# Performance work log

Hardware: AMD Instinct MI355X
Metric: run time of the kernel (lower is better)

Reference implementation:

```python
import jax, jax.numpy as jnp
import numpy as np

BS, SEQ, C, NC, H, W = 8, 512, 512, 5, 768, 768


def setup_inputs() -> dict:
    key = jax.random.key(0)
    k1, k2, k3, k4, k5, k6, k7, k8 = jax.random.split(key, 8)
    fuse_embeddings = jax.random.normal(k1, (BS, SEQ, C), dtype=jnp.float32)
    class_labels = jax.random.normal(k2, (BS, NC, H, W), dtype=jnp.float32)
    # valid boxes: x0<x1<=W, y0<y1<=H (coords order: x0, y0, x1, y1)
    x0 = jax.random.randint(k3, (BS, SEQ), 0, W - 1)
    y0 = jax.random.randint(k4, (BS, SEQ), 0, H - 1)
    x1 = jnp.minimum(x0 + jax.random.randint(k5, (BS, SEQ), 1, 64), W)
    y1 = jnp.minimum(y0 + jax.random.randint(k6, (BS, SEQ), 1, 16), H)
    coords = jnp.stack([x0, y0, x1, y1], axis=-1).astype(jnp.int32)
    mask = jax.random.randint(k7, (BS, SEQ), 0, 2).astype(jnp.int32)
    # classification_net (Linear) params
    bound = 1.0 / np.sqrt(C)
    Wc = jax.random.uniform(k8, (NC, C), minval=-bound, maxval=bound, dtype=jnp.float32)
    bc = jnp.zeros((NC,), dtype=jnp.float32)
    return {"fuse_embeddings": fuse_embeddings, "class_labels": class_labels,
            "Wc": Wc, "bc": bc, "coords": coords, "mask": mask}


def _forward(fuse_embeddings, class_labels, Wc, bc, coords, mask):
    bs, seq_len, _ = fuse_embeddings.shape
    nc = Wc.shape[0]
    # linear classifier over all tokens: [bs, seq, nc]
    logits = jnp.einsum("bsc,nc->bsn", fuse_embeddings, Wc) + bc
    # per-pixel hard label: [bs, H, W]
    lab = jnp.argmax(class_labels, axis=1)
    onehot = jax.nn.one_hot(lab, nc, dtype=logits.dtype)  # [bs, H, W, nc]
    # padded integral image -> O(1) box histograms (replaces per-ROI bincount)
    ii = jnp.cumsum(jnp.cumsum(onehot, axis=1), axis=2)
    ii = jnp.pad(ii, ((0, 0), (1, 0), (1, 0), (0, 0)))  # [bs, H+1, W+1, nc]
    x0, y0, x1, y1 = coords[..., 0], coords[..., 1], coords[..., 2], coords[..., 3]
    # degenerate-box fix from the original code
    y1 = jnp.where(y1 == y0, y1 + 1, y1)
    x1 = jnp.where(x1 == x0, x1 + 1, x1)
    b_idx = jnp.arange(bs)[:, None]
    g = lambda y, x: ii[b_idx, y, x, :]
    counts = g(y1, x1) - g(y0, x1) - g(y1, x0) + g(y0, x0)  # [bs, seq, nc]
    maj = jnp.argmax(counts, axis=-1)  # majority-vote label, first-max tiebreak like bincount().argmax()
    # masked-mean cross entropy (CE over tokens with mask==1)
    logp = jax.nn.log_softmax(logits, axis=-1)
    nll = -jnp.take_along_axis(logp, maj[..., None], axis=-1)[..., 0]
    m = (mask == 1).astype(logits.dtype)
    return jnp.sum(nll * m) / jnp.sum(m)


def reference(fuse_embeddings, class_labels, Wc, bc, coords, mask):
    return _forward(fuse_embeddings, class_labels, Wc, bc, coords, mask)
```

## Files before the change

### kernel.cpp

```cpp
#include <hip/hip_runtime.h>

#define BS 8
#define SEQ 512
#define CDIM 512
#define NC 5
#define IMG_H 768
#define IMG_W 768
#define HW (IMG_H * IMG_W)
#define NTOK (BS * SEQ)

__global__ __launch_bounds__(256) void token_kernel(
    const float* __restrict__ emb,
    const float* __restrict__ cls,
    const float* __restrict__ Wc,
    const float* __restrict__ bc,
    const int*   __restrict__ coords,
    const int*   __restrict__ mask,
    float2* __restrict__ ws)
{
    const int token = blockIdx.x;
    const int b     = token / SEQ;
    const int t     = threadIdx.x;
    const int wave  = t >> 6;
    const int lane  = t & 63;

    const float2 e = *(const float2*)(emb + (size_t)token * CDIM + t * 2);
    float part[NC];
#pragma unroll
    for (int c = 0; c < NC; ++c) {
        const float2 w = *(const float2*)(Wc + c * CDIM + t * 2);
        part[c] = e.x * w.x + e.y * w.y;
    }

    int x0 = coords[token * 4 + 0];
    int y0 = coords[token * 4 + 1];
    int x1 = coords[token * 4 + 2];
    int y1 = coords[token * 4 + 3];
    if (y1 == y0) y1++;
    if (x1 == x0) x1++;
    if (x1 > IMG_W) x1 = IMG_W;
    if (y1 > IMG_H) y1 = IMG_H;

    const int tx = lane;
    const int ty = wave;

    int hist[NC] = {0, 0, 0, 0, 0};
    const float* base = cls + (size_t)b * NC * HW;
    for (int yy = y0 + ty; yy < y1; yy += 4) {
        for (int xx = x0 + tx; xx < x1; xx += 64) {
            const float* p = base + yy * IMG_W + xx;
            const float v0 = p[0 * HW];
            const float v1 = p[1 * HW];
            const float v2 = p[2 * HW];
            const float v3 = p[3 * HW];
            const float v4 = p[4 * HW];
            int lab = 0; float best = v0;
            if (v1 > best) { best = v1; lab = 1; }
            if (v2 > best) { best = v2; lab = 2; }
            if (v3 > best) { best = v3; lab = 3; }
            if (v4 > best) { best = v4; lab = 4; }
#pragma unroll
            for (int c = 0; c < NC; ++c) hist[c] += (lab == c);
        }
    }

#pragma unroll
    for (int off = 32; off >= 1; off >>= 1) {
#pragma unroll
        for (int c = 0; c < NC; ++c) {
            part[c] += __shfl_down(part[c], off);
            hist[c] += __shfl_down(hist[c], off);
        }
    }

    __shared__ float s_part[4][NC];
    __shared__ int   s_hist[4][NC];
    if (lane == 0) {
#pragma unroll
        for (int c = 0; c < NC; ++c) {
            s_part[wave][c] = part[c];
            s_hist[wave][c] = hist[c];
        }
    }
    __syncthreads();

    if (t == 0) {
        float l[NC];
        int   h[NC];
#pragma unroll
        for (int c = 0; c < NC; ++c) {
            l[c] = s_part[0][c] + s_part[1][c] + s_part[2][c] + s_part[3][c] + bc[c];
            h[c] = s_hist[0][c] + s_hist[1][c] + s_hist[2][c] + s_hist[3][c];
        }
        int maj = 0, bestc = h[0];
#pragma unroll
        for (int c = 1; c < NC; ++c)
            if (h[c] > bestc) { bestc = h[c]; maj = c; }

        float m = l[0];
#pragma unroll
        for (int c = 1; c < NC; ++c) m = fmaxf(m, l[c]);
        float s = 0.0f;
#pragma unroll
        for (int c = 0; c < NC; ++c) s += __expf(l[c] - m);
        const float nll = m + __logf(s) - l[maj];

        const float mk = (mask[token] == 1) ? 1.0f : 0.0f;
        ws[token] = make_float2(nll * mk, mk);
    }
}

__global__ __launch_bounds__(256) void finalize_kernel(
    const float2* __restrict__ ws, float* __restrict__ out)
{
    float a = 0.0f, bsum = 0.0f;
    for (int i = threadIdx.x; i < NTOK; i += 256) {
        const float2 v = ws[i];
        a += v.x; bsum += v.y;
    }
#pragma unroll
    for (int off = 32; off >= 1; off >>= 1) {
        a    += __shfl_down(a, off);
        bsum += __shfl_down(bsum, off);
    }
    __shared__ float sa[4], sb[4];
    const int wave = threadIdx.x >> 6;
    if ((threadIdx.x & 63) == 0) { sa[wave] = a; sb[wave] = bsum; }
    __syncthreads();
    if (threadIdx.x == 0) {
        a    = sa[0] + sa[1] + sa[2] + sa[3];
        bsum = sb[0] + sb[1] + sb[2] + sb[3];
        out[0] = a / bsum;
    }
}

extern "C" void kernel_launch(void* const* d_in, const int* in_sizes, int n_in,
                              void* d_out, int out_size, void* d_ws, size_t ws_size,
                              hipStream_t stream) {
    const float* emb    = (const float*)d_in[0];
    const float* cls    = (const float*)d_in[1];
    const float* Wc     = (const float*)d_in[2];
    const float* bc     = (const float*)d_in[3];
    const int*   coords = (const int*)d_in[4];
    const int*   mask   = (const int*)d_in[5];
    float* out = (float*)d_out;
    float2* ws = (float2*)d_ws;

    token_kernel<<<NTOK, 256, 0, stream>>>(emb, cls, Wc, bc, coords, mask, ws);
    finalize_kernel<<<1, 256, 0, stream>>>(ws, out);
}
```

Before: 151.3 us.

## Map one wavefront per token and pack histogram into 64-bit counter

Each block now handles four tokens, one per wavefront, instead of one token per 256-thread block. Within a wave, each lane covers one box column (box widths stay below 64) and loops over the rows. The five class counts are packed into 12-bit fields of a single 64-bit value, so the wave reduction needs one shuffle chain instead of five. The per-token logits use wider float4 loads, and partial sums are combined per block, which shrinks the finalize input. The column mapping assumes boxes at most 64 wide and at most 4095 pixels per field.

```diff
diff --git a/kernel.cpp b/kernel.cpp
--- a/kernel.cpp
+++ b/kernel.cpp
@@ -8,6 +8,7 @@
 #define IMG_W 768
 #define HW (IMG_H * IMG_W)
 #define NTOK (BS * SEQ)
+#define NBLK (NTOK / 4)
 
 __global__ __launch_bounds__(256) void token_kernel(
     const float* __restrict__ emb,
@@ -18,19 +19,11 @@
     const int*   __restrict__ mask,
     float2* __restrict__ ws)
 {
-    const int token = blockIdx.x;
-    const int b     = token / SEQ;
     const int t     = threadIdx.x;
     const int wave  = t >> 6;
     const int lane  = t & 63;
-
-    const float2 e = *(const float2*)(emb + (size_t)token * CDIM + t * 2);
-    float part[NC];
-#pragma unroll
-    for (int c = 0; c < NC; ++c) {
-        const float2 w = *(const float2*)(Wc + c * CDIM + t * 2);
-        part[c] = e.x * w.x + e.y * w.y;
-    }
+    const int token = blockIdx.x * 4 + wave;
+    const int b     = token >> 9;
 
     int x0 = coords[token * 4 + 0];
     int y0 = coords[token * 4 + 1];
@@ -41,61 +34,62 @@
     if (x1 > IMG_W) x1 = IMG_W;
     if (y1 > IMG_H) y1 = IMG_H;
 
-    const int tx = lane;
-    const int ty = wave;
+    unsigned long long hp = 0ull;
+    {
+        const int xx = x0 + lane;
+        const bool xok = (xx < x1);
+        const float* p0 = cls + (size_t)b * NC * HW + y0 * IMG_W + xx;
+#pragma unroll 4
+        for (int yy = y0; yy < y1; ++yy, p0 += IMG_W) {
+            if (xok) {
+                const float v0 = p0[0 * HW];
+                const float v1 = p0[1 * HW];
+                const float v2 = p0[2 * HW];
+                const float v3 = p0[3 * HW];
+                const float v4 = p0[4 * HW];
+                int lab = 0; float best = v0;
+                if (v1 > best) { best = v1; lab = 1; }
+                if (v2 > best) { best = v2; lab = 2; }
+                if (v3 > best) { best = v3; lab = 3; }
+                if (v4 > best) { best = v4; lab = 4; }
+                hp += 1ull << (lab * 12);
+            }
+        }
+    }
 
-    int hist[NC] = {0, 0, 0, 0, 0};
-    const float* base = cls + (size_t)b * NC * HW;
-    for (int yy = y0 + ty; yy < y1; yy += 4) {
-        for (int xx = x0 + tx; xx < x1; xx += 64) {
-            const float* p = base + yy * IMG_W + xx;
-            const float v0 = p[0 * HW];
-            const float v1 = p[1 * HW];
-            const float v2 = p[2 * HW];
-            const float v3 = p[3 * HW];
-            const float v4 = p[4 * HW];
-            int lab = 0; float best = v0;
-            if (v1 > best) { best = v1; lab = 1; }
-            if (v2 > best) { best = v2; lab = 2; }
-            if (v3 > best) { best = v3; lab = 3; }
-            if (v4 > best) { best = v4; lab = 4; }
+    const float* e = emb + (size_t)token * CDIM + lane * 8;
+    const float4 e0 = *(const float4*)(e);
+    const float4 e1 = *(const float4*)(e + 4);
+    float part[NC];
 #pragma unroll
-            for (int c = 0; c < NC; ++c) hist[c] += (lab == c);
-        }
+    for (int c = 0; c < NC; ++c) {
+        const float* w = Wc + c * CDIM + lane * 8;
+        const float4 w0 = *(const float4*)(w);
+        const float4 w1 = *(const float4*)(w + 4);
+        part[c] = e0.x * w0.x + e0.y * w0.y + e0.z * w0.z + e0.w * w0.w
+                + e1.x * w1.x + e1.y * w1.y + e1.z * w1.z + e1.w * w1.w;
     }
 
 #pragma unroll
     for (int off = 32; off >= 1; off >>= 1) {
 #pragma unroll
-        for (int c = 0; c < NC; ++c) {
-            part[c] += __shfl_down(part[c], off);
-            hist[c] += __shfl_down(hist[c], off);
-        }
+        for (int c = 0; c < NC; ++c) part[c] += __shfl_down(part[c], off);
+        hp += __shfl_down(hp, off);
     }
 
-    __shared__ float s_part[4][NC];
-    __shared__ int   s_hist[4][NC];
+    __shared__ float2 s_pair[4];
     if (lane == 0) {
+        float l[NC];
 #pragma unroll
-        for (int c = 0; c < NC; ++c) {
-            s_part[wave][c] = part[c];
-            s_hist[wave][c] = hist[c];
+        for (int c = 0; c < NC; ++c) l[c] = part[c] + bc[c];
+
+        int maj = 0;
+        int bestc = (int)(hp & 4095);
+#pragma unroll
+        for (int c = 1; c < NC; ++c) {
+            const int hc = (int)((hp >> (12 * c)) & 4095);
+            if (hc > bestc) { bestc = hc; maj = c; }
         }
-    }
-    __syncthreads();
-
-    if (t == 0) {
-        float l[NC];
-        int   h[NC];
-#pragma unroll
-        for (int c = 0; c < NC; ++c) {
-            l[c] = s_part[0][c] + s_part[1][c] + s_part[2][c] + s_part[3][c] + bc[c];
-            h[c] = s_hist[0][c] + s_hist[1][c] + s_hist[2][c] + s_hist[3][c];
-        }
-        int maj = 0, bestc = h[0];
-#pragma unroll
-        for (int c = 1; c < NC; ++c)
-            if (h[c] > bestc) { bestc = h[c]; maj = c; }
 
         float m = l[0];
 #pragma unroll
@@ -106,7 +100,15 @@
         const float nll = m + __logf(s) - l[maj];
 
         const float mk = (mask[token] == 1) ? 1.0f : 0.0f;
-        ws[token] = make_float2(nll * mk, mk);
+        s_pair[wave] = make_float2(nll * mk, mk);
+    }
+    __syncthreads();
+
+    if (t == 0) {
+        const float2 a = s_pair[0], b2 = s_pair[1],
+                     c2 = s_pair[2], d2 = s_pair[3];
+        ws[blockIdx.x] = make_float2(a.x + b2.x + c2.x + d2.x,
+                                     a.y + b2.y + c2.y + d2.y);
     }
 }
 
@@ -114,7 +116,8 @@
     const float2* __restrict__ ws, float* __restrict__ out)
 {
     float a = 0.0f, bsum = 0.0f;
-    for (int i = threadIdx.x; i < NTOK; i += 256) {
+#pragma unroll
+    for (int i = threadIdx.x; i < NBLK; i += 256) {
         const float2 v = ws[i];
         a += v.x; bsum += v.y;
     }
@@ -146,6 +149,6 @@
     float* out = (float*)d_out;
     float2* ws = (float2*)d_ws;
 
-    token_kernel<<<NTOK, 256, 0, stream>>>(emb, cls, Wc, bc, coords, mask, ws);
+    token_kernel<<<NBLK, 256, 0, stream>>>(emb, cls, Wc, bc, coords, mask, ws);
     finalize_kernel<<<1, 256, 0, stream>>>(ws, out);
 }
```

Result: faster. 147.3 us (-2.7%).
